# Performance work log

Measured on AMD Instinct MI355X. Metric: run time of the kernel, lower is better.

The kernel has to match this reference:

```python
import jax, jax.numpy as jnp
import numpy as np

NUM_USERS = 100000
NUM_RATINGS = 5
EMBED_DIM = 64
ATT_DIM = 16
B, G, L, S = 16384, 8, 50, 32


def setup_inputs() -> dict:
    key = jax.random.key(0)
    ks = jax.random.split(key, 16)
    inp = {
        # forward args (int / bool constants)
        "nodes": jax.random.randint(ks[0], (B, G), 0, NUM_USERS),
        "history_u": jax.random.randint(ks[1], (B, L), 0, NUM_USERS),
        "history_r": jax.random.randint(ks[2], (B, L), 0, NUM_RATINGS),
        "history_mask": jax.random.randint(ks[3], (B, L), 0, 2).astype(bool).at[:, 0].set(True),
        "social_adj": jax.random.randint(ks[4], (B, S), 0, NUM_USERS),
        "social_mask": jax.random.randint(ks[5], (B, S), 0, 2).astype(bool).at[:, 0].set(True),
        # learned parameters
        "features": jax.random.normal(ks[6], (NUM_USERS, EMBED_DIM), jnp.float32) * 0.02,
        "r_embed": jax.random.normal(ks[7], (NUM_RATINGS, EMBED_DIM), jnp.float32) * 0.02,
        "wg1": jax.random.normal(ks[8], (EMBED_DIM, ATT_DIM), jnp.float32) / np.sqrt(EMBED_DIM),
        "bg1": jnp.zeros((ATT_DIM,), jnp.float32),
        "wg2": jax.random.normal(ks[9], (ATT_DIM, 1), jnp.float32) / np.sqrt(ATT_DIM),
        "bg2": jnp.zeros((1,), jnp.float32),
        "w1": jax.random.normal(ks[10], (2 * EMBED_DIM, EMBED_DIM), jnp.float32) / np.sqrt(2 * EMBED_DIM),
        "b1": jnp.zeros((EMBED_DIM,), jnp.float32),
    }
    return inp


def _masked_mean(x, mask):
    # x: [B, N, D], mask: [B, N] float -> [B, D]
    denom = jnp.maximum(mask.sum(axis=1, keepdims=True), 1.0)
    return (x * mask[..., None]).sum(axis=1) / denom


def reference(nodes, history_u, history_r, history_mask, social_adj, social_mask,
              features, r_embed, wg1, bg1, wg2, bg2, w1, b1):
    dt = features.dtype
    # --- Group_Embedding: attention pooling over member embeddings ---
    members = features[nodes]                              # [B, G, D] gather
    h = jnp.tanh(members @ wg1 + bg1)                      # [B, G, 16]
    logits = (h @ wg2 + bg2)[..., 0]                       # [B, G]
    alpha = jax.nn.softmax(logits, axis=-1)
    self_feats = jnp.einsum('bg,bgd->bd', alpha, members)  # [B, D]

    # --- aggregator: ragged history (item+rating) + social neighbor means ---
    hm = history_mask.astype(dt)
    hist = features[history_u] + r_embed[history_r]        # [B, L, D] gather
    hist_mean = _masked_mean(hist, hm)                     # [B, D]

    sm = social_mask.astype(dt)
    soc_mean = _masked_mean(features[social_adj], sm)      # [B, D]

    neigh_feats = 0.5 * (hist_mean + soc_mean)             # [B, D]

    # --- concat -> linear -> relu ---
    combined = jnp.concatenate([self_feats, neigh_feats], axis=1)  # [B, 2D]
    return jax.nn.relu(combined @ w1 + b1)                 # [B, D]
```

## Files before the change

### kernel.cpp

```cpp
#include <hip/hip_runtime.h>
#include <cstdint>
#include <cstddef>

#define BB 16384

__global__ __launch_bounds__(256) void k_fused(
    const int* __restrict__ nodes, const int* __restrict__ hist_u,
    const int* __restrict__ hist_r, const int* __restrict__ hist_m,
    const int* __restrict__ soc_a, const int* __restrict__ soc_m,
    const float* __restrict__ features, const float* __restrict__ r_embed,
    const float* __restrict__ wg1, const float* __restrict__ bg1,
    const float* __restrict__ wg2, const float* __restrict__ bg2,
    const float* __restrict__ w1, const float* __restrict__ b1,
    float* __restrict__ out)
{
    __shared__ float wg1t[16 * 68];
    __shared__ float mrow[4][8 * 68];
    __shared__ int   lcomp[4][96];
    __shared__ float wcomp[4][96];
    __shared__ float combs[4][128];

    const int tid  = threadIdx.x;
    const int lane = tid & 63;
    const int wv   = tid >> 6;
    const int e    = blockIdx.x * 4 + wv;
    const int sub  = lane & 15;
    const int grp  = lane >> 4;
    const char* fB = (const char*)features;

    {
        const float4 w = ((const float4*)wg1)[tid];
        const int d = tid >> 2, k0 = (tid & 3) * 4;
        wg1t[(k0 + 0) * 68 + d] = w.x;
        wg1t[(k0 + 1) * 68 + d] = w.y;
        wg1t[(k0 + 2) * 68 + d] = w.z;
        wg1t[(k0 + 3) * 68 + d] = w.w;
    }

    lcomp[wv][lane] = 0;
    wcomp[wv][lane] = 0.f;
    if (lane < 32) { lcomp[wv][64 + lane] = 0; wcomp[wv][64 + lane] = 0.f; }

    const float4* re4p = (const float4*)r_embed;
    const float4 re0 = re4p[0 * 16 + sub];
    const float4 re1 = re4p[1 * 16 + sub];
    const float4 re2 = re4p[2 * 16 + sub];
    const float4 re3 = re4p[3 * 16 + sub];
    const float4 re4 = re4p[4 * 16 + sub];

    int nd = (lane < 8) ? nodes[e * 8 + lane] : 0;
    int hu = 0, hr = 0, hmv = 0;
    if (lane < 50) {
        hu  = hist_u[e * 50 + lane];
        hr  = hist_r[e * 50 + lane];
        hmv = hist_m[e * 50 + lane];
    }
    int sa = 0, sk = 0;
    if (lane < 32) {
        sa = soc_a[e * 32 + lane];
        sk = soc_m[e * 32 + lane];
    }

    uint64_t hb = __ballot(hmv != 0);
    const int hc = (int)__popcll(hb);
    int hrank = (int)__popcll(hb & ((1ull << lane) - 1));

    uint64_t sbm = __ballot(sk != 0);
    const int scn = (int)__popcll(sbm);
    int srank = (int)__popcll(sbm & ((1ull << lane) - 1));

    const float ih = 1.f / (float)hc;
    const float is = 1.f / (float)scn;
    const float hw = 0.5f * ih;
    const float sw = 0.5f * is;

    if (hmv) { lcomp[wv][hrank] = hu << 8; wcomp[wv][hrank] = hw; }
    if (sk)  { lcomp[wv][hc + srank] = sa << 8; wcomp[wv][hc + srank] = sw; }

    const int c0 = (int)__popcll(__ballot(hmv && hr == 0));
    const int c1 = (int)__popcll(__ballot(hmv && hr == 1));
    const int c2 = (int)__popcll(__ballot(hmv && hr == 2));
    const int c3 = (int)__popcll(__ballot(hmv && hr == 3));
    const int c4 = (int)__popcll(__ballot(hmv && hr == 4));

    const int u0 = __shfl(nd, grp);
    const int u1 = __shfl(nd, 4 + grp);
    const float4 v0 = *(const float4*)(fB + ((unsigned)u0 << 8) + sub * 16);
    const float4 v1 = *(const float4*)(fB + ((unsigned)u1 << 8) + sub * 16);
    *(float4*)&mrow[wv][grp * 68 + sub * 4]       = v0;
    *(float4*)&mrow[wv][(4 + grp) * 68 + sub * 4] = v1;

    __syncthreads();

    float h0, h1;
    {
        const int k = sub;
        const float bk = bg1[k];
        h0 = bk; h1 = bk;
        #pragma unroll
        for (int d4 = 0; d4 < 16; ++d4) {
            const float4 wk = *(const float4*)&wg1t[k * 68 + d4 * 4];
            const float4 m0 = *(const float4*)&mrow[wv][grp * 68 + d4 * 4];
            const float4 m1 = *(const float4*)&mrow[wv][(4 + grp) * 68 + d4 * 4];
            h0 += m0.x * wk.x + m0.y * wk.y + m0.z * wk.z + m0.w * wk.w;
            h1 += m1.x * wk.x + m1.y * wk.y + m1.z * wk.z + m1.w * wk.w;
        }
        const float wk2 = wg2[k];
        float x0 = fminf(fmaxf(h0, -9.f), 9.f);
        float x1 = fminf(fmaxf(h1, -9.f), 9.f);
        float e20 = __expf(2.f * x0), e21 = __expf(2.f * x1);
        h0 = (e20 - 1.f) / (e20 + 1.f) * wk2;
        h1 = (e21 - 1.f) / (e21 + 1.f) * wk2;
        h0 += __shfl_xor(h0, 1); h1 += __shfl_xor(h1, 1);
        h0 += __shfl_xor(h0, 2); h1 += __shfl_xor(h1, 2);
        h0 += __shfl_xor(h0, 4); h1 += __shfl_xor(h1, 4);
        h0 += __shfl_xor(h0, 8); h1 += __shfl_xor(h1, 8);
    }
    const float bg2v = bg2[0];
    const float l0 = h0 + bg2v;
    const float l1 = h1 + bg2v;

    float mx = fmaxf(l0, l1);
    mx = fmaxf(mx, __shfl_xor(mx, 16));
    mx = fmaxf(mx, __shfl_xor(mx, 32));
    float e0 = __expf(l0 - mx), e1 = __expf(l1 - mx);
    float s = e0 + e1;
    s += __shfl_xor(s, 16);
    s += __shfl_xor(s, 32);
    const float a0 = e0 / s, a1 = e1 / s;

    float4 sf4;
    sf4.x = a0 * v0.x + a1 * v1.x;
    sf4.y = a0 * v0.y + a1 * v1.y;
    sf4.z = a0 * v0.z + a1 * v1.z;
    sf4.w = a0 * v0.w + a1 * v1.w;

    int   pkA = lcomp[wv][lane];
    int   pkB = lcomp[wv][64 + (lane & 31)];
    float wgA = wcomp[wv][lane];
    float wgB = wcomp[wv][64 + (lane & 31)];
    const int n = hc + scn;

    float4 nb4 = {0.f, 0.f, 0.f, 0.f};
    for (int base = 0; base < n; base += 16) {
        #pragma unroll
        for (int j = 0; j < 4; ++j) {
            const int cbase = base + j * 4;
            int off; float w;
            if (cbase < 64) {
                off = __shfl(pkA, cbase + grp);
                w   = __shfl(wgA, cbase + grp);
            } else {
                off = __shfl(pkB, cbase - 64 + grp);
                w   = __shfl(wgB, cbase - 64 + grp);
            }
            const float4 v = *(const float4*)(fB + (unsigned)off + sub * 16);
            nb4.x += w * v.x; nb4.y += w * v.y;
            nb4.z += w * v.z; nb4.w += w * v.w;
        }
    }

#define XRED(v4)                                            \
    v4.x += __shfl_xor(v4.x, 16); v4.x += __shfl_xor(v4.x, 32); \
    v4.y += __shfl_xor(v4.y, 16); v4.y += __shfl_xor(v4.y, 32); \
    v4.z += __shfl_xor(v4.z, 16); v4.z += __shfl_xor(v4.z, 32); \
    v4.w += __shfl_xor(v4.w, 16); v4.w += __shfl_xor(v4.w, 32);
    XRED(sf4)
    XRED(nb4)
#undef XRED

    float f0 = hw * (float)c0, f1 = hw * (float)c1, f2 = hw * (float)c2,
          f3 = hw * (float)c3, f4 = hw * (float)c4;
    nb4.x += f0 * re0.x + f1 * re1.x + f2 * re2.x + f3 * re3.x + f4 * re4.x;
    nb4.y += f0 * re0.y + f1 * re1.y + f2 * re2.y + f3 * re3.y + f4 * re4.y;
    nb4.z += f0 * re0.z + f1 * re1.z + f2 * re2.z + f3 * re3.z + f4 * re4.z;
    nb4.w += f0 * re0.w + f1 * re1.w + f2 * re2.w + f3 * re3.w + f4 * re4.w;

    if (grp == 0) *(float4*)&combs[wv][sub * 4] = sf4;
    if (grp == 1) *(float4*)&combs[wv][64 + sub * 4] = nb4;

    const int col = lane;
    float y = b1[col];
    #pragma unroll 8
    for (int k4 = 0; k4 < 32; ++k4) {
        const float4 c = *(const float4*)&combs[wv][k4 * 4];
        y += c.x * w1[(k4 * 4 + 0) * 64 + col]
           + c.y * w1[(k4 * 4 + 1) * 64 + col]
           + c.z * w1[(k4 * 4 + 2) * 64 + col]
           + c.w * w1[(k4 * 4 + 3) * 64 + col];
    }
    out[(size_t)e * 64 + col] = fmaxf(y, 0.f);
}

extern "C" void kernel_launch(void* const* d_in, const int* in_sizes, int n_in,
                              void* d_out, int out_size, void* d_ws, size_t ws_size,
                              hipStream_t stream)
{
    const int*   nodes    = (const int*)d_in[0];
    const int*   hu       = (const int*)d_in[1];
    const int*   hr       = (const int*)d_in[2];
    const int*   hm       = (const int*)d_in[3];
    const int*   sa       = (const int*)d_in[4];
    const int*   smk      = (const int*)d_in[5];
    const float* features = (const float*)d_in[6];
    const float* r_embed  = (const float*)d_in[7];
    const float* wg1      = (const float*)d_in[8];
    const float* bg1      = (const float*)d_in[9];
    const float* wg2      = (const float*)d_in[10];
    const float* bg2      = (const float*)d_in[11];
    const float* w1       = (const float*)d_in[12];
    const float* b1       = (const float*)d_in[13];
    float* out = (float*)d_out;

    (void)d_ws; (void)ws_size;

    k_fused<<<BB / 4, 256, 0, stream>>>(nodes, hu, hr, hm, sa, smk,
                                        features, r_embed, wg1, bg1, wg2, bg2,
                                        w1, b1, out);
}
```

Measured before the change: 140.3 us.

## Prefetch first neighbor gathers before attention and shrink LDS footprint

Moves the block-wide barrier to right after the wg1 transpose, so each wave can then proceed on its own. The first 16 neighbor feature gathers are issued before the attention math so their latency overlaps with it. The per-entry weight array is dropped and weights are recomputed from hc/scn, and the member rows share a single reused scratch buffer. A min-waves hint of 6 is added to __launch_bounds__. Together these aim at higher occupancy and better latency hiding on the gather-bound path, in exchange for more live registers and a possible spill risk under the occupancy hint.

```diff
diff --git a/kernel.cpp b/kernel.cpp
--- a/kernel.cpp
+++ b/kernel.cpp
@@ -4,7 +4,7 @@
 
 #define BB 16384
 
-__global__ __launch_bounds__(256) void k_fused(
+__global__ __launch_bounds__(256, 6) void k_fused(
     const int* __restrict__ nodes, const int* __restrict__ hist_u,
     const int* __restrict__ hist_r, const int* __restrict__ hist_m,
     const int* __restrict__ soc_a, const int* __restrict__ soc_m,
@@ -15,10 +15,8 @@
     float* __restrict__ out)
 {
     __shared__ float wg1t[16 * 68];
-    __shared__ float mrow[4][8 * 68];
     __shared__ int   lcomp[4][96];
-    __shared__ float wcomp[4][96];
-    __shared__ float combs[4][128];
+    __shared__ float scratch[4][272];
 
     const int tid  = threadIdx.x;
     const int lane = tid & 63;
@@ -36,10 +34,23 @@
         wg1t[(k0 + 2) * 68 + d] = w.z;
         wg1t[(k0 + 3) * 68 + d] = w.w;
     }
+    __syncthreads();
 
     lcomp[wv][lane] = 0;
-    wcomp[wv][lane] = 0.f;
-    if (lane < 32) { lcomp[wv][64 + lane] = 0; wcomp[wv][64 + lane] = 0.f; }
+    if (lane < 32) lcomp[wv][64 + lane] = 0;
+
+    int nd = (lane < 8) ? nodes[e * 8 + lane] : 0;
+    int hu = 0, hr = 0, hmv = 0;
+    if (lane < 50) {
+        hu  = hist_u[e * 50 + lane];
+        hr  = hist_r[e * 50 + lane];
+        hmv = hist_m[e * 50 + lane];
+    }
+    int sa = 0, sk = 0;
+    if (lane < 32) {
+        sa = soc_a[e * 32 + lane];
+        sk = soc_m[e * 32 + lane];
+    }
 
     const float4* re4p = (const float4*)r_embed;
     const float4 re0 = re4p[0 * 16 + sub];
@@ -48,19 +59,6 @@
     const float4 re3 = re4p[3 * 16 + sub];
     const float4 re4 = re4p[4 * 16 + sub];
 
-    int nd = (lane < 8) ? nodes[e * 8 + lane] : 0;
-    int hu = 0, hr = 0, hmv = 0;
-    if (lane < 50) {
-        hu  = hist_u[e * 50 + lane];
-        hr  = hist_r[e * 50 + lane];
-        hmv = hist_m[e * 50 + lane];
-    }
-    int sa = 0, sk = 0;
-    if (lane < 32) {
-        sa = soc_a[e * 32 + lane];
-        sk = soc_m[e * 32 + lane];
-    }
-
     uint64_t hb = __ballot(hmv != 0);
     const int hc = (int)__popcll(hb);
     int hrank = (int)__popcll(hb & ((1ull << lane) - 1));
@@ -69,13 +67,12 @@
     const int scn = (int)__popcll(sbm);
     int srank = (int)__popcll(sbm & ((1ull << lane) - 1));
 
-    const float ih = 1.f / (float)hc;
-    const float is = 1.f / (float)scn;
-    const float hw = 0.5f * ih;
-    const float sw = 0.5f * is;
-
-    if (hmv) { lcomp[wv][hrank] = hu << 8; wcomp[wv][hrank] = hw; }
-    if (sk)  { lcomp[wv][hc + srank] = sa << 8; wcomp[wv][hc + srank] = sw; }
+    const float hw = 0.5f / (float)hc;
+    const float sw = 0.5f / (float)scn;
+    const int   n  = hc + scn;
+
+    if (hmv) lcomp[wv][hrank] = hu << 8;
+    if (sk)  lcomp[wv][hc + srank] = sa << 8;
 
     const int c0 = (int)__popcll(__ballot(hmv && hr == 0));
     const int c1 = (int)__popcll(__ballot(hmv && hr == 1));
@@ -83,29 +80,43 @@
     const int c3 = (int)__popcll(__ballot(hmv && hr == 3));
     const int c4 = (int)__popcll(__ballot(hmv && hr == 4));
 
+    int pkA = lcomp[wv][lane];
+    int pkB = lcomp[wv][64 + (lane & 31)];
+
     const int u0 = __shfl(nd, grp);
     const int u1 = __shfl(nd, 4 + grp);
     const float4 v0 = *(const float4*)(fB + ((unsigned)u0 << 8) + sub * 16);
     const float4 v1 = *(const float4*)(fB + ((unsigned)u1 << 8) + sub * 16);
-    *(float4*)&mrow[wv][grp * 68 + sub * 4]       = v0;
-    *(float4*)&mrow[wv][(4 + grp) * 68 + sub * 4] = v1;
-
-    __syncthreads();
-
-    float h0, h1;
+
+    const int o0 = __shfl(pkA, 0  + grp);
+    const int o1 = __shfl(pkA, 4  + grp);
+    const int o2 = __shfl(pkA, 8  + grp);
+    const int o3 = __shfl(pkA, 12 + grp);
+    const float4 g0 = *(const float4*)(fB + (unsigned)o0 + sub * 16);
+    const float4 g1 = *(const float4*)(fB + (unsigned)o1 + sub * 16);
+    const float4 g2 = *(const float4*)(fB + (unsigned)o2 + sub * 16);
+    const float4 g3 = *(const float4*)(fB + (unsigned)o3 + sub * 16);
+
+    const float bg1v = bg1[sub];
+    const float wk2  = wg2[sub];
+    float h0 = bg1v, h1 = bg1v;
+
+    *(float4*)&scratch[wv][grp * 68 + sub * 4] = v0;
+    #pragma unroll
+    for (int d4 = 0; d4 < 16; ++d4) {
+        const float4 m  = *(const float4*)&scratch[wv][grp * 68 + d4 * 4];
+        const float4 wk = *(const float4*)&wg1t[sub * 68 + d4 * 4];
+        h0 += m.x * wk.x + m.y * wk.y + m.z * wk.z + m.w * wk.w;
+    }
+    *(float4*)&scratch[wv][grp * 68 + sub * 4] = v1;
+    #pragma unroll
+    for (int d4 = 0; d4 < 16; ++d4) {
+        const float4 m  = *(const float4*)&scratch[wv][grp * 68 + d4 * 4];
+        const float4 wk = *(const float4*)&wg1t[sub * 68 + d4 * 4];
+        h1 += m.x * wk.x + m.y * wk.y + m.z * wk.z + m.w * wk.w;
+    }
+
     {
-        const int k = sub;
-        const float bk = bg1[k];
-        h0 = bk; h1 = bk;
-        #pragma unroll
-        for (int d4 = 0; d4 < 16; ++d4) {
-            const float4 wk = *(const float4*)&wg1t[k * 68 + d4 * 4];
-            const float4 m0 = *(const float4*)&mrow[wv][grp * 68 + d4 * 4];
-            const float4 m1 = *(const float4*)&mrow[wv][(4 + grp) * 68 + d4 * 4];
-            h0 += m0.x * wk.x + m0.y * wk.y + m0.z * wk.z + m0.w * wk.w;
-            h1 += m1.x * wk.x + m1.y * wk.y + m1.z * wk.z + m1.w * wk.w;
-        }
-        const float wk2 = wg2[k];
         float x0 = fminf(fmaxf(h0, -9.f), 9.f);
         float x1 = fminf(fmaxf(h1, -9.f), 9.f);
         float e20 = __expf(2.f * x0), e21 = __expf(2.f * x1);
@@ -135,25 +146,27 @@
     sf4.z = a0 * v0.z + a1 * v1.z;
     sf4.w = a0 * v0.w + a1 * v1.w;
 
-    int   pkA = lcomp[wv][lane];
-    int   pkB = lcomp[wv][64 + (lane & 31)];
-    float wgA = wcomp[wv][lane];
-    float wgB = wcomp[wv][64 + (lane & 31)];
-    const int n = hc + scn;
-
     float4 nb4 = {0.f, 0.f, 0.f, 0.f};
-    for (int base = 0; base < n; base += 16) {
+    {
+        const float w0 = (0  + grp < hc) ? hw : ((0  + grp < n) ? sw : 0.f);
+        const float w1q= (4  + grp < hc) ? hw : ((4  + grp < n) ? sw : 0.f);
+        const float w2 = (8  + grp < hc) ? hw : ((8  + grp < n) ? sw : 0.f);
+        const float w3 = (12 + grp < hc) ? hw : ((12 + grp < n) ? sw : 0.f);
+        nb4.x += w0 * g0.x + w1q * g1.x + w2 * g2.x + w3 * g3.x;
+        nb4.y += w0 * g0.y + w1q * g1.y + w2 * g2.y + w3 * g3.y;
+        nb4.z += w0 * g0.z + w1q * g1.z + w2 * g2.z + w3 * g3.z;
+        nb4.w += w0 * g0.w + w1q * g1.w + w2 * g2.w + w3 * g3.w;
+    }
+
+    for (int base = 16; base < n; base += 16) {
         #pragma unroll
         for (int j = 0; j < 4; ++j) {
             const int cbase = base + j * 4;
-            int off; float w;
-            if (cbase < 64) {
-                off = __shfl(pkA, cbase + grp);
-                w   = __shfl(wgA, cbase + grp);
-            } else {
-                off = __shfl(pkB, cbase - 64 + grp);
-                w   = __shfl(wgB, cbase - 64 + grp);
-            }
+            int off;
+            if (cbase < 64) off = __shfl(pkA, cbase + grp);
+            else            off = __shfl(pkB, cbase - 64 + grp);
+            const int idx = cbase + grp;
+            const float w = (idx < hc) ? hw : ((idx < n) ? sw : 0.f);
             const float4 v = *(const float4*)(fB + (unsigned)off + sub * 16);
             nb4.x += w * v.x; nb4.y += w * v.y;
             nb4.z += w * v.z; nb4.w += w * v.w;
@@ -176,14 +189,14 @@
     nb4.z += f0 * re0.z + f1 * re1.z + f2 * re2.z + f3 * re3.z + f4 * re4.z;
     nb4.w += f0 * re0.w + f1 * re1.w + f2 * re2.w + f3 * re3.w + f4 * re4.w;
 
-    if (grp == 0) *(float4*)&combs[wv][sub * 4] = sf4;
-    if (grp == 1) *(float4*)&combs[wv][64 + sub * 4] = nb4;
+    if (grp == 0) *(float4*)&scratch[wv][sub * 4] = sf4;
+    if (grp == 1) *(float4*)&scratch[wv][64 + sub * 4] = nb4;
 
     const int col = lane;
     float y = b1[col];
     #pragma unroll 8
     for (int k4 = 0; k4 < 32; ++k4) {
-        const float4 c = *(const float4*)&combs[wv][k4 * 4];
+        const float4 c = *(const float4*)&scratch[wv][k4 * 4];
         y += c.x * w1[(k4 * 4 + 0) * 64 + col]
            + c.y * w1[(k4 * 4 + 1) * 64 + col]
            + c.z * w1[(k4 * 4 + 2) * 64 + col]
```

Result: slower. 197.6 us (+40.8%).
